# Optimization experiments

Hardware: AMD Instinct MI355X
Metric: run time of the kernel (lower is better)

Reference implementation:

```python
import jax, jax.numpy as jnp
import numpy as np

# Irrep layout: blocks of (multiplicity, l); identical for input and output.
LS = [0, 1, 2, 3]
MULS = [64, 64, 64, 64]
N = 65536
DIM = sum(m * (2 * l + 1) for m, l in zip(MULS, LS))  # 1024
NPATH = len(LS) * len(LS)  # 16 valid (l_out, l_in) paths
MAXM = max(LS)             # max |m| over all paths
NW = sum(mo * mi for mo in MULS for mi in MULS)  # 65536 path weights


def _split_blocks(x):
    """Split flat irrep vector into per-block [n, mul, 2l+1] views."""
    blocks, off = [], 0
    for mul, l in zip(MULS, LS):
        d = mul * (2 * l + 1)
        blocks.append(x[:, off:off + d].reshape(x.shape[0], mul, 2 * l + 1))
        off += d
    return blocks


def setup_inputs() -> dict:
    key = jax.random.key(0)
    k = jax.random.split(key, 5)
    return {
        "x": jax.random.normal(k[0], (N, DIM), jnp.float32),
        "weights": jax.random.normal(k[1], (NW,), jnp.float32) * 0.1,
        "hzero": jax.random.normal(k[2], (NPATH,), jnp.float32),
        "hpos": jax.random.normal(k[3], (NPATH, MAXM), jnp.float32),
        "hneg": jax.random.normal(k[4], (NPATH, MAXM), jnp.float32),
    }


def reference(x, weights, hzero, hpos, hneg):
    xb = _split_blocks(x)
    n = x.shape[0]
    outb = [jnp.zeros((n, mul, 2 * l + 1), x.dtype) for mul, l in zip(MULS, LS)]
    p, off = 0, 0
    for oi, (mo, lo) in enumerate(zip(MULS, LS)):
        for ii, (mi, li) in enumerate(zip(MULS, LS)):
            W = weights[off:off + mo * mi].reshape(mo, mi)
            off += mo * mi
            xi = xb[ii]  # [n, mi, 2*li+1]
            # m = 0 component
            y0 = jnp.einsum('nm,om->no', xi[:, :, li], W) * hzero[p]
            outb[oi] = outb[oi].at[:, :, lo].add(y0)
            # |m| >= 1: O(2)-reduced pos/neg mixing with Wigner-derived couplings
            for m in range(1, min(lo, li) + 1):
                hp, hn = hpos[p, m - 1], hneg[p, m - 1]
                xp, xn = xi[:, :, li + m], xi[:, :, li - m]
                outb[oi] = outb[oi].at[:, :, lo + m].add(
                    jnp.einsum('nm,om->no', hp * xp + hn * xn, W))
                outb[oi] = outb[oi].at[:, :, lo - m].add(
                    jnp.einsum('nm,om->no', hp * xn - hn * xp, W))
            p += 1
    return jnp.concatenate([b.reshape(n, -1) for b in outb], axis=1)
```

## Files before the change

### kernel.cpp

```cpp
#include <hip/hip_runtime.h>


typedef __attribute__((ext_vector_type(8))) short bhalf8_t;
typedef __attribute__((ext_vector_type(4))) float f32x4_t;

#define NROWS 65536
#define DIMV  1024

#define M0_OFF 0
#define M1_OFF 65536
#define M2_OFF 212992
#define M3_OFF 278528
#define M_TOTAL 294912

#define OP 1028

__device__ __forceinline__ short f2bf(float f) {
    unsigned u = __builtin_bit_cast(unsigned, f);
    u = (u + 0x7FFFu + ((u >> 16) & 1u)) >> 16;
    return (short)u;
}

__global__ __launch_bounds__(256) void build_M(const float* __restrict__ w,
                                               const float* __restrict__ hz,
                                               const float* __restrict__ hp,
                                               const float* __restrict__ hn,
                                               short* __restrict__ M) {
    int idx = blockIdx.x * 256 + threadIdx.x;
    if (idx >= M_TOTAL) return;

    int m, A, B;
    if (idx < M1_OFF)      { m = 0; int lo = idx;            A = lo / 256u; B = lo - A * 256; }
    else if (idx < M2_OFF) { m = 1; int lo = idx - M1_OFF;   A = lo / 384u; B = lo - A * 384; }
    else if (idx < M3_OFF) { m = 2; int lo = idx - M2_OFF;   A = lo / 256u; B = lo - A * 256; }
    else                   { m = 3; int lo = idx - M3_OFF;   A = lo / 128u; B = lo - A * 128; }

    int ob, so, o, ib, si, i;
    if (m == 0) { ob = A >> 6;       so = 0;            o = A & 63;
                  ib = B >> 6;       si = 0;            i = B & 63; }
    else        { ob = (A >> 7) + m; so = (A >> 6) & 1; o = A & 63;
                  ib = (B >> 7) + m; si = (B >> 6) & 1; i = B & 63; }

    int p = ob * 4 + ib;
    float wv = w[p * 4096 + o * 64 + i];
    float coef;
    if (m == 0) {
        coef = hz[p];
    } else {
        float hpv = hp[p * 3 + (m - 1)];
        float hnv = hn[p * 3 + (m - 1)];
        coef = (so == 0) ? ((si == 0) ? hpv : hnv)
                         : ((si == 0) ? -hnv : hpv);
    }
    M[idx] = f2bf(wv * coef);
}

__global__ __launch_bounds__(1024) void tp_main(const float* __restrict__ x,
                                                const short* __restrict__ Mall,
                                                float* __restrict__ out) {
    __shared__ __align__(16) char smem[16 * OP * 4];
    short* __restrict__ xbuf = (short*)smem;
    float* __restrict__ obuf = (float*)smem;

    const int tid  = threadIdx.x;
    const int lane = tid & 63;
    const int lr   = lane & 15;
    const int q    = lane >> 4;
    const int wv   = tid >> 6;
    const int rowbase = blockIdx.x << 6;

    int m, cb;
    if (wv < 4)       { m = 0; cb = wv << 6; }
    else if (wv < 10) { m = 1; cb = (wv - 4) << 6; }
    else if (wv < 14) { m = 2; cb = (wv - 10) << 6; }
    else              { m = 3; cb = (wv - 14) << 6; }
    const int Wm   = (m == 1) ? 384 : ((m == 3) ? 128 : 256);
    const int Moff = (m == 0) ? M0_OFF : (m == 1) ? M1_OFF : (m == 2) ? M2_OFF : M3_OFF;
    const short* __restrict__ Mg = Mall + Moff;

    f32x4_t acc[4][4];
#pragma unroll
    for (int c = 0; c < 4; ++c)
#pragma unroll
        for (int r = 0; r < 4; ++r)
            acc[c][r] = (f32x4_t){0.f, 0.f, 0.f, 0.f};

#pragma unroll
    for (int ii = 0; ii < 4; ++ii) {
        const int l   = ii;
        const int nch = 2 * l + 1;
        const int d4  = 16 * nch;
        const int RS  = nch * 72;
        const int bo  = 64 * l * l;

        __syncthreads();

#pragma unroll
        for (int e = 0; e < nch; ++e) {
            int id  = e * 1024 + tid;
            int row = id / d4;
            int cc  = id - row * d4;
            int col = cc * 4;
            const float4 v = *(const float4*)(x + (size_t)(rowbase + row) * DIMV + bo + col);
            short* dst = &xbuf[row * RS];
            { int ci = col;     int i = ci / nch; int ji = ci - i * nch; dst[ji * 72 + i] = f2bf(v.x); }
            { int ci = col + 1; int i = ci / nch; int ji = ci - i * nch; dst[ji * 72 + i] = f2bf(v.y); }
            { int ci = col + 2; int i = ci / nch; int ji = ci - i * nch; dst[ji * 72 + i] = f2bf(v.z); }
            { int ci = col + 3; int i = ci / nch; int ji = ci - i * nch; dst[ji * 72 + i] = f2bf(v.w); }
        }
        __syncthreads();

        if (m <= l) {
            const int nsi = (m == 0) ? 1 : 2;
            for (int si = 0; si < nsi; ++si) {
                const int ji    = l + ((si == 0) ? m : -m);
                const int kbase = ((m == 0) ? (ii << 6) : (((ii - m) << 7) + (si << 6)));
#pragma unroll
                for (int kk = 0; kk < 2; ++kk) {
                    bhalf8_t a[4];
                    const int eo = ji * 72 + kk * 32 + q * 8;
#pragma unroll
                    for (int r = 0; r < 4; ++r)
                        a[r] = *(const bhalf8_t*)&xbuf[(r * 16 + lr) * RS + eo];
                    const int ko = kbase + kk * 32 + q * 8;
#pragma unroll
                    for (int c = 0; c < 4; ++c) {
                        const bhalf8_t b = *(const bhalf8_t*)&Mg[(cb + c * 16 + lr) * Wm + ko];
#pragma unroll
                        for (int r = 0; r < 4; ++r)
                            acc[c][r] = __builtin_amdgcn_mfma_f32_16x16x32_bf16(
                                a[r], b, acc[c][r], 0, 0, 0);
                    }
                }
            }
        }
    }

    int origc[4];
#pragma unroll
    for (int c = 0; c < 4; ++c) {
        const int P = cb + c * 16 + lr;
        int ob, o, jo;
        if (m == 0) { ob = P >> 6;       o = P & 63; jo = ob; }
        else        { ob = (P >> 7) + m; o = P & 63;
                      jo = ob + ((((P >> 6) & 1) == 0) ? m : -m); }
        origc[c] = 64 * ob * ob + o * (2 * ob + 1) + jo;
    }

#pragma unroll
    for (int r = 0; r < 4; ++r) {
        __syncthreads();
#pragma unroll
        for (int c = 0; c < 4; ++c) {
#pragma unroll
            for (int g = 0; g < 4; ++g)
                obuf[(q * 4 + g) * OP + origc[c]] = acc[c][r][g];
        }
        __syncthreads();
#pragma unroll
        for (int it = 0; it < 4; ++it) {
            const int j   = it * 1024 + tid;
            const int row = j >> 8;
            const int c4  = (j & 255) << 2;
            const float4 v = *(const float4*)&obuf[row * OP + c4];
            *(float4*)&out[(size_t)(rowbase + r * 16 + row) * DIMV + c4] = v;
        }
    }
}

extern "C" void kernel_launch(void* const* d_in, const int* in_sizes, int n_in,
                              void* d_out, int out_size, void* d_ws, size_t ws_size,
                              hipStream_t stream) {
    const float* x   = (const float*)d_in[0];
    const float* wts = (const float*)d_in[1];
    const float* hz  = (const float*)d_in[2];
    const float* hp  = (const float*)d_in[3];
    const float* hn  = (const float*)d_in[4];
    float* out = (float*)d_out;
    short* M   = (short*)d_ws;

    build_M<<<dim3(M_TOTAL / 256), dim3(256), 0, stream>>>(wts, hz, hp, hn, M);
    tp_main<<<dim3(NROWS / 64), dim3(1024), 0, stream>>>(x, M, out);
}
```

Before: 514.3 us.

## Double-buffer x staging across irrep blocks with smaller 512-thread blocks

Each block now covers 32 rows with 8 waves instead of 64 rows with 16 waves. Each wave handles 128 output columns and 2 row tiles, where it used to handle 64 columns and 4 row tiles. The x staging for irrep block l+1 is written into a second LDS buffer while MFMA compute runs on block l, so global loads overlap the matrix work and one barrier per stage is removed. The trade-offs are that each wave now reads twice as many M operand rows per block, twice as many blocks load M overall, and the shared-memory footprint still limits how many blocks fit per CU.

Result: slower. 583.1 us (+13.4%).

```diff
diff --git a/kernel.cpp b/kernel.cpp
--- a/kernel.cpp
+++ b/kernel.cpp
@@ -6,6 +6,8 @@
 
 #define NROWS 65536
 #define DIMV  1024
+#define NT    512
+#define RPW   32
 
 #define M0_OFF 0
 #define M1_OFF 65536
@@ -14,6 +16,8 @@
 #define M_TOTAL 294912
 
 #define OP 1028
+
+#define XB1_OFF 11520
 
 __device__ __forceinline__ short f2bf(float f) {
     unsigned u = __builtin_bit_cast(unsigned, f);
@@ -55,11 +59,66 @@
     M[idx] = f2bf(wv * coef);
 }
 
-__global__ __launch_bounds__(1024) void tp_main(const float* __restrict__ x,
-                                                const short* __restrict__ Mall,
-                                                float* __restrict__ out) {
+template<int L>
+__device__ __forceinline__ void stage_block(const float* __restrict__ x, int rowbase,
+                                            short* __restrict__ xb, int tid) {
+    constexpr int nch = 2 * L + 1;
+    constexpr int d4  = 16 * nch;
+    constexpr int RS  = nch * 72;
+    constexpr int bo  = 64 * L * L;
+#pragma unroll
+    for (int e = 0; e < nch; ++e) {
+        int id  = e * NT + tid;
+        int row = id / d4;
+        int cc  = id - row * d4;
+        int col = cc * 4;
+        const float4 v = *(const float4*)(x + (size_t)(rowbase + row) * DIMV + bo + col);
+        short* dst = &xb[row * RS];
+        { int ci = col;     int i = ci / nch; int ji = ci - i * nch; dst[ji * 72 + i] = f2bf(v.x); }
+        { int ci = col + 1; int i = ci / nch; int ji = ci - i * nch; dst[ji * 72 + i] = f2bf(v.y); }
+        { int ci = col + 2; int i = ci / nch; int ji = ci - i * nch; dst[ji * 72 + i] = f2bf(v.z); }
+        { int ci = col + 3; int i = ci / nch; int ji = ci - i * nch; dst[ji * 72 + i] = f2bf(v.w); }
+    }
+}
+
+template<int L>
+__device__ __forceinline__ void compute_block(const short* __restrict__ xb,
+                                              const short* __restrict__ Mg,
+                                              int m, int Wm, int cb, int lr, int q,
+                                              f32x4_t acc[8][2]) {
+    if (m > L) return;
+    constexpr int nch = 2 * L + 1;
+    constexpr int RS  = nch * 72;
+    const int nsi = (m == 0) ? 1 : 2;
+    for (int si = 0; si < nsi; ++si) {
+        const int ji    = L + ((si == 0) ? m : -m);
+        const int kbase = (m == 0) ? (L << 6) : (((L - m) << 7) + (si << 6));
+#pragma unroll
+        for (int kk = 0; kk < 2; ++kk) {
+            bhalf8_t a[2];
+            const int eo = ji * 72 + kk * 32 + q * 8;
+#pragma unroll
+            for (int r = 0; r < 2; ++r)
+                a[r] = *(const bhalf8_t*)&xb[(r * 16 + lr) * RS + eo];
+            const int ko = kbase + kk * 32 + q * 8;
+#pragma unroll
+            for (int c = 0; c < 8; ++c) {
+                const bhalf8_t b = *(const bhalf8_t*)&Mg[(cb + c * 16 + lr) * Wm + ko];
+#pragma unroll
+                for (int r = 0; r < 2; ++r)
+                    acc[c][r] = __builtin_amdgcn_mfma_f32_16x16x32_bf16(
+                        a[r], b, acc[c][r], 0, 0, 0);
+            }
+        }
+    }
+}
+
+__global__ __launch_bounds__(NT, 4) void tp_main(const float* __restrict__ x,
+                                                 const short* __restrict__ Mall,
+                                                 float* __restrict__ out) {
     __shared__ __align__(16) char smem[16 * OP * 4];
-    short* __restrict__ xbuf = (short*)smem;
+    short* __restrict__ xb0  = (short*)smem;
+    short* __restrict__ xb1  = (short*)smem + XB1_OFF;
     float* __restrict__ obuf = (float*)smem;
 
     const int tid  = threadIdx.x;
@@ -67,78 +126,45 @@
     const int lr   = lane & 15;
     const int q    = lane >> 4;
     const int wv   = tid >> 6;
-    const int rowbase = blockIdx.x << 6;
+    const int rowbase = blockIdx.x * RPW;
 
     int m, cb;
-    if (wv < 4)       { m = 0; cb = wv << 6; }
-    else if (wv < 10) { m = 1; cb = (wv - 4) << 6; }
-    else if (wv < 14) { m = 2; cb = (wv - 10) << 6; }
-    else              { m = 3; cb = (wv - 14) << 6; }
+    if      (wv < 2) { m = 0; cb = wv << 7; }
+    else if (wv < 5) { m = 1; cb = (wv - 2) << 7; }
+    else if (wv < 7) { m = 2; cb = (wv - 5) << 7; }
+    else             { m = 3; cb = 0; }
     const int Wm   = (m == 1) ? 384 : ((m == 3) ? 128 : 256);
     const int Moff = (m == 0) ? M0_OFF : (m == 1) ? M1_OFF : (m == 2) ? M2_OFF : M3_OFF;
     const short* __restrict__ Mg = Mall + Moff;
 
-    f32x4_t acc[4][4];
-#pragma unroll
-    for (int c = 0; c < 4; ++c)
-#pragma unroll
-        for (int r = 0; r < 4; ++r)
+    f32x4_t acc[8][2];
+#pragma unroll
+    for (int c = 0; c < 8; ++c)
+#pragma unroll
+        for (int r = 0; r < 2; ++r)
             acc[c][r] = (f32x4_t){0.f, 0.f, 0.f, 0.f};
 
-#pragma unroll
-    for (int ii = 0; ii < 4; ++ii) {
-        const int l   = ii;
-        const int nch = 2 * l + 1;
-        const int d4  = 16 * nch;
-        const int RS  = nch * 72;
-        const int bo  = 64 * l * l;
-
-        __syncthreads();
-
-#pragma unroll
-        for (int e = 0; e < nch; ++e) {
-            int id  = e * 1024 + tid;
-            int row = id / d4;
-            int cc  = id - row * d4;
-            int col = cc * 4;
-            const float4 v = *(const float4*)(x + (size_t)(rowbase + row) * DIMV + bo + col);
-            short* dst = &xbuf[row * RS];
-            { int ci = col;     int i = ci / nch; int ji = ci - i * nch; dst[ji * 72 + i] = f2bf(v.x); }
-            { int ci = col + 1; int i = ci / nch; int ji = ci - i * nch; dst[ji * 72 + i] = f2bf(v.y); }
-            { int ci = col + 2; int i = ci / nch; int ji = ci - i * nch; dst[ji * 72 + i] = f2bf(v.z); }
-            { int ci = col + 3; int i = ci / nch; int ji = ci - i * nch; dst[ji * 72 + i] = f2bf(v.w); }
-        }
-        __syncthreads();
-
-        if (m <= l) {
-            const int nsi = (m == 0) ? 1 : 2;
-            for (int si = 0; si < nsi; ++si) {
-                const int ji    = l + ((si == 0) ? m : -m);
-                const int kbase = ((m == 0) ? (ii << 6) : (((ii - m) << 7) + (si << 6)));
-#pragma unroll
-                for (int kk = 0; kk < 2; ++kk) {
-                    bhalf8_t a[4];
-                    const int eo = ji * 72 + kk * 32 + q * 8;
-#pragma unroll
-                    for (int r = 0; r < 4; ++r)
-                        a[r] = *(const bhalf8_t*)&xbuf[(r * 16 + lr) * RS + eo];
-                    const int ko = kbase + kk * 32 + q * 8;
-#pragma unroll
-                    for (int c = 0; c < 4; ++c) {
-                        const bhalf8_t b = *(const bhalf8_t*)&Mg[(cb + c * 16 + lr) * Wm + ko];
-#pragma unroll
-                        for (int r = 0; r < 4; ++r)
-                            acc[c][r] = __builtin_amdgcn_mfma_f32_16x16x32_bf16(
-                                a[r], b, acc[c][r], 0, 0, 0);
-                    }
-                }
-            }
-        }
-    }
-
-    int origc[4];
-#pragma unroll
-    for (int c = 0; c < 4; ++c) {
+    stage_block<0>(x, rowbase, xb0, tid);
+    __syncthreads();
+
+    stage_block<1>(x, rowbase, xb1, tid);
+    compute_block<0>(xb0, Mg, m, Wm, cb, lr, q, acc);
+    __syncthreads();
+
+    stage_block<2>(x, rowbase, xb0, tid);
+    compute_block<1>(xb1, Mg, m, Wm, cb, lr, q, acc);
+    __syncthreads();
+
+    stage_block<3>(x, rowbase, xb1, tid);
+    compute_block<2>(xb0, Mg, m, Wm, cb, lr, q, acc);
+    __syncthreads();
+
+    compute_block<3>(xb1, Mg, m, Wm, cb, lr, q, acc);
+    __syncthreads();
+
+    int origc[8];
+#pragma unroll
+    for (int c = 0; c < 8; ++c) {
         const int P = cb + c * 16 + lr;
         int ob, o, jo;
         if (m == 0) { ob = P >> 6;       o = P & 63; jo = ob; }
@@ -148,23 +174,23 @@
     }
 
 #pragma unroll
-    for (int r = 0; r < 4; ++r) {
-        __syncthreads();
-#pragma unroll
-        for (int c = 0; c < 4; ++c) {
+    for (int r2 = 0; r2 < 2; ++r2) {
+#pragma unroll
+        for (int c = 0; c < 8; ++c) {
 #pragma unroll
             for (int g = 0; g < 4; ++g)
-                obuf[(q * 4 + g) * OP + origc[c]] = acc[c][r][g];
+                obuf[(q * 4 + g) * OP + origc[c]] = acc[c][r2][g];
         }
         __syncthreads();
 #pragma unroll
-        for (int it = 0; it < 4; ++it) {
-            const int j   = it * 1024 + tid;
+        for (int it = 0; it < 8; ++it) {
+            const int j   = it * NT + tid;
             const int row = j >> 8;
             const int c4  = (j & 255) << 2;
             const float4 v = *(const float4*)&obuf[row * OP + c4];
-            *(float4*)&out[(size_t)(rowbase + r * 16 + row) * DIMV + c4] = v;
+            *(float4*)&out[(size_t)(rowbase + r2 * 16 + row) * DIMV + c4] = v;
         }
+        __syncthreads();
     }
 }
 
@@ -180,5 +206,5 @@
     short* M   = (short*)d_ws;
 
     build_M<<<dim3(M_TOTAL / 256), dim3(256), 0, stream>>>(wts, hz, hp, hn, M);
-    tp_main<<<dim3(NROWS / 64), dim3(1024), 0, stream>>>(x, M, out);
-}
+    tp_main<<<dim3(NROWS / RPW), dim3(NT), 0, stream>>>(x, M, out);
+}
```

## Stage all irrep blocks into LDS at once, then run all MFMA passes

Applied to the files above, without the earlier changes.

Gives each l-block of the input tile its own LDS region, loads and converts all four blocks up front, then runs the MFMA compute for every block behind a single barrier. Before, staging and compute alternated with two barriers per block. The aim is to remove those intermediate barriers and issue all global loads together for more memory-level parallelism. In exchange, LDS per workgroup grows to 144 KB, which likely drops residency to one 1024-thread block per CU, leaving less latency hiding across blocks.

Result: slower. 528.7 us (+2.8%).

```diff
diff --git a/kernel.cpp b/kernel.cpp
--- a/kernel.cpp
+++ b/kernel.cpp
@@ -6,6 +6,8 @@
 
 #define NROWS 65536
 #define DIMV  1024
+#define NT    1024
+#define RPW   64
 
 #define M0_OFF 0
 #define M1_OFF 65536
@@ -14,6 +16,10 @@
 #define M_TOTAL 294912
 
 #define OP 1028
+
+__device__ __forceinline__ constexpr int xoff(int L) {
+    return (L == 0) ? 0 : (L == 1) ? 4608 : (L == 2) ? 18432 : 41472;
+}
 
 __device__ __forceinline__ short f2bf(float f) {
     unsigned u = __builtin_bit_cast(unsigned, f);
@@ -55,10 +61,64 @@
     M[idx] = f2bf(wv * coef);
 }
 
-__global__ __launch_bounds__(1024) void tp_main(const float* __restrict__ x,
-                                                const short* __restrict__ Mall,
-                                                float* __restrict__ out) {
-    __shared__ __align__(16) char smem[16 * OP * 4];
+template<int L>
+__device__ __forceinline__ void stage_block(const float* __restrict__ x, int rowbase,
+                                            short* __restrict__ xb, int tid) {
+    constexpr int nch = 2 * L + 1;
+    constexpr int d4  = 16 * nch;
+    constexpr int RS  = nch * 72;
+    constexpr int bo  = 64 * L * L;
+#pragma unroll
+    for (int e = 0; e < nch; ++e) {
+        int id  = e * NT + tid;
+        int row = id / d4;
+        int cc  = id - row * d4;
+        int col = cc * 4;
+        const float4 v = *(const float4*)(x + (size_t)(rowbase + row) * DIMV + bo + col);
+        short* dst = &xb[row * RS];
+        { int ci = col;     int i = ci / nch; int ji = ci - i * nch; dst[ji * 72 + i] = f2bf(v.x); }
+        { int ci = col + 1; int i = ci / nch; int ji = ci - i * nch; dst[ji * 72 + i] = f2bf(v.y); }
+        { int ci = col + 2; int i = ci / nch; int ji = ci - i * nch; dst[ji * 72 + i] = f2bf(v.z); }
+        { int ci = col + 3; int i = ci / nch; int ji = ci - i * nch; dst[ji * 72 + i] = f2bf(v.w); }
+    }
+}
+
+template<int L>
+__device__ __forceinline__ void compute_block(const short* __restrict__ xb,
+                                              const short* __restrict__ Mg,
+                                              int m, int Wm, int cb, int lr, int q,
+                                              f32x4_t (&acc)[4][4]) {
+    if (m > L) return;
+    constexpr int nch = 2 * L + 1;
+    constexpr int RS  = nch * 72;
+    const int nsi = (m == 0) ? 1 : 2;
+    for (int si = 0; si < nsi; ++si) {
+        const int ji    = L + ((si == 0) ? m : -m);
+        const int kbase = (m == 0) ? (L << 6) : (((L - m) << 7) + (si << 6));
+#pragma unroll
+        for (int kk = 0; kk < 2; ++kk) {
+            bhalf8_t a[4];
+            const int eo = ji * 72 + kk * 32 + q * 8;
+#pragma unroll
+            for (int r = 0; r < 4; ++r)
+                a[r] = *(const bhalf8_t*)&xb[(r * 16 + lr) * RS + eo];
+            const int ko = kbase + kk * 32 + q * 8;
+#pragma unroll
+            for (int c = 0; c < 4; ++c) {
+                const bhalf8_t b = *(const bhalf8_t*)&Mg[(cb + c * 16 + lr) * Wm + ko];
+#pragma unroll
+                for (int r = 0; r < 4; ++r)
+                    acc[c][r] = __builtin_amdgcn_mfma_f32_16x16x32_bf16(
+                        a[r], b, acc[c][r], 0, 0, 0);
+            }
+        }
+    }
+}
+
+__global__ __launch_bounds__(NT) void tp_main(const float* __restrict__ x,
+                                              const short* __restrict__ Mall,
+                                              float* __restrict__ out) {
+    __shared__ __align__(16) char smem[147456];
     short* __restrict__ xbuf = (short*)smem;
     float* __restrict__ obuf = (float*)smem;
 
@@ -67,7 +127,7 @@
     const int lr   = lane & 15;
     const int q    = lane >> 4;
     const int wv   = tid >> 6;
-    const int rowbase = blockIdx.x << 6;
+    const int rowbase = blockIdx.x * RPW;
 
     int m, cb;
     if (wv < 4)       { m = 0; cb = wv << 6; }
@@ -85,56 +145,16 @@
         for (int r = 0; r < 4; ++r)
             acc[c][r] = (f32x4_t){0.f, 0.f, 0.f, 0.f};
 
-#pragma unroll
-    for (int ii = 0; ii < 4; ++ii) {
-        const int l   = ii;
-        const int nch = 2 * l + 1;
-        const int d4  = 16 * nch;
-        const int RS  = nch * 72;
-        const int bo  = 64 * l * l;
-
-        __syncthreads();
-
-#pragma unroll
-        for (int e = 0; e < nch; ++e) {
-            int id  = e * 1024 + tid;
-            int row = id / d4;
-            int cc  = id - row * d4;
-            int col = cc * 4;
-            const float4 v = *(const float4*)(x + (size_t)(rowbase + row) * DIMV + bo + col);
-            short* dst = &xbuf[row * RS];
-            { int ci = col;     int i = ci / nch; int ji = ci - i * nch; dst[ji * 72 + i] = f2bf(v.x); }
-            { int ci = col + 1; int i = ci / nch; int ji = ci - i * nch; dst[ji * 72 + i] = f2bf(v.y); }
-            { int ci = col + 2; int i = ci / nch; int ji = ci - i * nch; dst[ji * 72 + i] = f2bf(v.z); }
-            { int ci = col + 3; int i = ci / nch; int ji = ci - i * nch; dst[ji * 72 + i] = f2bf(v.w); }
-        }
-        __syncthreads();
-
-        if (m <= l) {
-            const int nsi = (m == 0) ? 1 : 2;
-            for (int si = 0; si < nsi; ++si) {
-                const int ji    = l + ((si == 0) ? m : -m);
-                const int kbase = ((m == 0) ? (ii << 6) : (((ii - m) << 7) + (si << 6)));
-#pragma unroll
-                for (int kk = 0; kk < 2; ++kk) {
-                    bhalf8_t a[4];
-                    const int eo = ji * 72 + kk * 32 + q * 8;
-#pragma unroll
-                    for (int r = 0; r < 4; ++r)
-                        a[r] = *(const bhalf8_t*)&xbuf[(r * 16 + lr) * RS + eo];
-                    const int ko = kbase + kk * 32 + q * 8;
-#pragma unroll
-                    for (int c = 0; c < 4; ++c) {
-                        const bhalf8_t b = *(const bhalf8_t*)&Mg[(cb + c * 16 + lr) * Wm + ko];
-#pragma unroll
-                        for (int r = 0; r < 4; ++r)
-                            acc[c][r] = __builtin_amdgcn_mfma_f32_16x16x32_bf16(
-                                a[r], b, acc[c][r], 0, 0, 0);
-                    }
-                }
-            }
-        }
-    }
+    stage_block<0>(x, rowbase, xbuf + xoff(0), tid);
+    stage_block<1>(x, rowbase, xbuf + xoff(1), tid);
+    stage_block<2>(x, rowbase, xbuf + xoff(2), tid);
+    stage_block<3>(x, rowbase, xbuf + xoff(3), tid);
+    __syncthreads();
+
+    compute_block<0>(xbuf + xoff(0), Mg, m, Wm, cb, lr, q, acc);
+    compute_block<1>(xbuf + xoff(1), Mg, m, Wm, cb, lr, q, acc);
+    compute_block<2>(xbuf + xoff(2), Mg, m, Wm, cb, lr, q, acc);
+    compute_block<3>(xbuf + xoff(3), Mg, m, Wm, cb, lr, q, acc);
 
     int origc[4];
 #pragma unroll
@@ -159,7 +179,7 @@
         __syncthreads();
 #pragma unroll
         for (int it = 0; it < 4; ++it) {
-            const int j   = it * 1024 + tid;
+            const int j   = it * NT + tid;
             const int row = j >> 8;
             const int c4  = (j & 255) << 2;
             const float4 v = *(const float4*)&obuf[row * OP + c4];
@@ -180,5 +200,5 @@
     short* M   = (short*)d_ws;
 
     build_M<<<dim3(M_TOTAL / 256), dim3(256), 0, stream>>>(wts, hz, hp, hn, M);
-    tp_main<<<dim3(NROWS / 64), dim3(1024), 0, stream>>>(x, M, out);
-}
+    tp_main<<<dim3(NROWS / RPW), dim3(NT), 0, stream>>>(x, M, out);
+}
```
